# Kernel optimization log

Hardware: AMD Instinct MI355X
Metric: run time of the kernel (lower is better)

Reference implementation:

```python
import jax, jax.numpy as jnp
import numpy as np

H = 128   # d_model / features
N = 32    # kept complex modes (d_state=64 -> 32 conjugate pairs)
B = 8
L = 8192


def setup_inputs() -> dict:
    key = jax.random.key(0)
    ks = jax.random.split(key, 8)
    x = jax.random.normal(ks[0], (B, H, L), jnp.float32)
    # S4D (diagonal SSM) kernel parameters; channels=2 for bidirectional
    C_re = (jax.random.normal(ks[1], (2, H, N), jnp.float32) * (0.5 ** 0.5))
    C_im = (jax.random.normal(ks[2], (2, H, N), jnp.float32) * (0.5 ** 0.5))
    log_A_real = jnp.log(0.5 * jnp.ones((H, N), jnp.float32))          # S4D-Lin init
    A_imag = jnp.tile(np.pi * jnp.arange(N, dtype=jnp.float32), (H, 1))
    # log_dt uniform in [log(1e-3), log(1e-1)]
    u = jax.random.uniform(ks[3], (H,), jnp.float32)
    log_dt = u * (np.log(0.1) - np.log(0.001)) + np.log(0.001)
    D = jax.random.normal(ks[4], (H,), jnp.float32)                    # skip term
    W_pw = jax.random.normal(ks[5], (H, H), jnp.float32) / np.sqrt(H)  # 1x1 conv weight (out, in)
    gamma = jnp.ones((H,), jnp.float32)
    beta = jnp.zeros((H,), jnp.float32)
    return {"x": x, "C_re": C_re, "C_im": C_im, "log_A_real": log_A_real,
            "A_imag": A_imag, "log_dt": log_dt, "D": D, "W_pw": W_pw,
            "gamma": gamma, "beta": beta}


def reference(x, C_re, C_im, log_A_real, A_imag, log_dt, D, W_pw, gamma, beta):
    Lx = x.shape[-1]
    # ---- S4D SSM kernel via Vandermonde (ZOH discretization) ----
    A = -jnp.exp(log_A_real) + 1j * A_imag                 # (H, N) complex
    dt = jnp.exp(log_dt)[:, None]                          # (H, 1)
    dtA = A * dt                                           # (H, N)
    C = C_re + 1j * C_im                                   # (2, H, N)
    Kc = C * ((jnp.exp(dtA) - 1.0) / A)                    # (2, H, N)
    vand = jnp.exp(dtA[:, :, None] * jnp.arange(Lx))       # (H, N, L)
    k = 2.0 * jnp.einsum('chn,hnl->chl', Kc, vand).real    # (2, H, L)
    # ---- bidirectional: causal half + anticausal (flipped) half ----
    k_full = (jnp.pad(k[0], ((0, 0), (0, Lx)))
              + jnp.pad(k[1][:, ::-1], ((0, 0), (Lx, 0))))  # (H, 2L)
    # ---- FFT convolution ----
    n = 2 * Lx
    y = jnp.fft.irfft(jnp.fft.rfft(x, n=n) * jnp.fft.rfft(k_full, n=n), n=n)[..., :Lx]
    y = y + x * D[:, None]                                 # skip connection
    y = jax.nn.gelu(y, approximate=False)                  # FFTConv default activation
    # ---- pointwise 1x1 conv (no bias) ----
    y = jnp.einsum('bhl,oh->bol', y, W_pw)
    # ---- BatchNorm1d (training-mode batch statistics) ----
    mean = jnp.mean(y, axis=(0, 2), keepdims=True)
    var = jnp.var(y, axis=(0, 2), keepdims=True)
    y = (y - mean) * jax.lax.rsqrt(var + 1e-5) * gamma[:, None] + beta[:, None]
    # ---- ELU + residual (dropout p=0) ----
    return jax.nn.elu(y) + x
```

## Files before the change

### kernel.cpp

```cpp
#include <hip/hip_runtime.h>
#include <math.h>

#define HCH   128
#define NMODE 32
#define BB    8
#define LLEN  8192
#define LC    256
#define CCH   (LLEN / LC)
#define ROWS  (BB * HCH)

typedef unsigned int uint;
typedef _Float16 f16x8 __attribute__((ext_vector_type(8)));
typedef float    f32x4 __attribute__((ext_vector_type(4)));

static __device__ __forceinline__ uint pk2(float a, float b) {
    union { _Float16 h[2]; uint u; } v;
    v.h[0] = (_Float16)a; v.h[1] = (_Float16)b;
    return v.u;
}

static __device__ __forceinline__ void cpow8(float wr, float wi, int e, float& pr, float& pi) {
    pr = 1.f; pi = 0.f;
    float br = wr, bi = wi;
    #pragma unroll
    for (int k = 0; k < 8; k++) {
        if (e & (1 << k)) { float t = pr * br - pi * bi; pi = pr * bi + pi * br; pr = t; }
        float t2 = br * br - bi * bi; bi = 2.f * br * bi; br = t2;
    }
}

__device__ __forceinline__ float gelu_f(float y) {
    float z = fabsf(y) * 0.7071067811865476f;
    float p = fmaf(z, 0.078108f, 0.000972f);
    p = fmaf(z, p, 0.230389f);
    p = fmaf(z, p, 0.278393f);
    p = fmaf(z, p, 1.0f);
    float p2 = p * p;
    float p4 = p2 * p2;
    float er = 1.f - __builtin_amdgcn_rcpf(p4);
    float s  = copysignf(er, y);
    return 0.5f * y * (1.f + s);
}

#define DPP_ADD(v, ctrl) { int _t = __builtin_amdgcn_update_dpp(0, __float_as_int(v), \
                             (ctrl), 0xF, 0xF, true); (v) += __int_as_float(_t); }

__global__ __launch_bounds__(256) void k_prep(const float* __restrict__ C_re,
                                              const float* __restrict__ C_im,
                                              const float* __restrict__ logA,
                                              const float* __restrict__ Aim,
                                              const float* __restrict__ logdt,
                                              _Float16* __restrict__ aT,
                                              _Float16* __restrict__ eT,
                                              float* __restrict__ Pw,
                                              float* __restrict__ stats) {
    __shared__ float wrL[32], wiL[32];
    __shared__ float G0r[32], G0i[32], G1r[32], G1i[32], H0r[32], H0i[32];
    __shared__ float k0L[256], k1L[256];
    int tid = threadIdx.x;
    int h = blockIdx.x;
    if (blockIdx.x == 0) stats[tid] = 0.f;
    if (tid < 32) {
        int n = tid, idx = h * 32 + n;
        float ar = expf(logA[idx]);
        float ai = Aim[idx];
        float dt = expf(logdt[h]);
        float dre = -ar * dt, dim = ai * dt;
        float er = expf(dre);
        float wr = er * cosf(dim), wi = er * sinf(dim);
        wrL[n] = wr; wiL[n] = wi;
        float eL = expf(dre * 256.f);
        Pw[idx]        = eL * cosf(dim * 256.f);
        Pw[4096 + idx] = eL * sinf(dim * 256.f);
        float den  = ar * ar + ai * ai;
        float numr = -(wr - 1.f) * ar + wi * ai;
        float numi = -wi * ar - (wr - 1.f) * ai;
        float Kr = numr / den, Ki = numi / den;
        float c0r = C_re[idx],        c0i = C_im[idx];
        float c1r = C_re[4096 + idx], c1i = C_im[4096 + idx];
        float g0r = 2.f * (c0r * Kr - c0i * Ki), g0i = 2.f * (c0r * Ki + c0i * Kr);
        G0r[n] = g0r; G0i[n] = g0i;
        G1r[n] = 2.f * (c1r * Kr - c1i * Ki);
        G1i[n] = 2.f * (c1r * Ki + c1i * Kr);
        H0r[n] = g0r * wr - g0i * wi;
        H0i[n] = g0r * wi + g0i * wr;
    }
    __syncthreads();
    {
        int tau = tid;
        float s0 = 0.f, s1 = 0.f;
        for (int n = 0; n < 32; n++) {
            float pr, pi2; cpow8(wrL[n], wiL[n], tau, pr, pi2);
            s0 += G0r[n] * pr - G0i[n] * pi2;
            s1 += G1r[n] * pr - G1i[n] * pi2;
        }
        k0L[tau] = s0; k1L[tau] = s1;
    }
    __syncthreads();
    for (int idx = tid; idx < 256 * 128; idx += 256) {
        int t  = idx >> 7;
        int sp = (idx & 127) << 1;
        float v0 = (sp     <= t) ? k0L[t - sp]     : k1L[sp - t - 1];
        float v1 = (sp + 1 <= t) ? k0L[t - sp - 1] : k1L[sp - t];
        *(uint*)&aT[((size_t)(h * 256 + t)) * 384 + sp] = pk2(v0, v1);
    }
    {
        int t = tid;
        size_t rb = ((size_t)(h * 256 + t)) * 384;
        for (int n = 0; n < 32; n++) {
            float wtr, wti, wur, wui;
            cpow8(wrL[n], wiL[n], t, wtr, wti);
            cpow8(wrL[n], wiL[n], 255 - t, wur, wui);
            float v0r = H0r[n] * wtr - H0i[n] * wti;
            float v0i = -(H0r[n] * wti + H0i[n] * wtr);
            float v1r = G1r[n] * wur - G1i[n] * wui;
            float v1i = -(G1r[n] * wui + G1i[n] * wur);
            *(uint*)&aT[rb + 256 + 2 * n] = pk2(v0r, v0i);
            *(uint*)&aT[rb + 320 + 2 * n] = pk2(v1r, v1i);
        }
    }
    for (int idx = tid; idx < 32 * 256; idx += 256) {
        int n = idx >> 8, s = idx & 255;
        float ar, ai2, br, bi2;
        cpow8(wrL[n], wiL[n], 255 - s, ar, ai2);
        cpow8(wrL[n], wiL[n], s, br, bi2);
        size_t base = (size_t)h * 128 * 256;
        eT[base + (size_t)(2 * n) * 256 + s]      = (_Float16)ar;
        eT[base + (size_t)(2 * n + 1) * 256 + s]  = (_Float16)ai2;
        eT[base + (size_t)(64 + 2 * n) * 256 + s] = (_Float16)br;
        eT[base + (size_t)(65 + 2 * n) * 256 + s] = (_Float16)bi2;
    }
}

__global__ __launch_bounds__(256, 2) void k_states_g(const float* __restrict__ x,
                                                     const _Float16* __restrict__ eT,
                                                     float* __restrict__ S_end) {
    __shared__ _Float16 At[128 * 40];
    __shared__ _Float16 Bt[128 * 40];
    int tid = threadIdx.x;
    int bid = blockIdx.x;
    int h = bid >> 1, mt = bid & 1;
    int wave = tid >> 6, lane = tid & 63;
    int wm = wave >> 1, wn = wave & 1;
    int lrow = lane & 15, quad = lane >> 4;
    int koff = quad * 8;
    f32x4 acc[4][4];
    #pragma unroll
    for (int a = 0; a < 4; a++)
        #pragma unroll
        for (int b = 0; b < 4; b++) acc[a][b] = (f32x4){0.f, 0.f, 0.f, 0.f};

    for (int kk = 0; kk < 256; kk += 32) {
        __syncthreads();
        #pragma unroll
        for (int i = 0; i < 4; i++) {
            int idx = tid + i * 256;
            int r = idx >> 3, seg = idx & 7;
            int bc = mt * 128 + r;
            const float* xp = x + (((size_t)((bc >> 5) * HCH + h)) << 13) + ((bc & 31) << 8) + kk + seg * 4;
            float4 v = *(const float4*)xp;
            uint2 o; o.x = pk2(v.x, v.y); o.y = pk2(v.z, v.w);
            *(uint2*)&At[r * 40 + seg * 4] = o;
        }
        #pragma unroll
        for (int i = 0; i < 2; i++) {
            int idx = tid + i * 256;
            int r = idx >> 2, sg = idx & 3;
            uint4 v = *(const uint4*)(eT + ((size_t)(h * 128 + r)) * 256 + kk + sg * 8);
            *(uint4*)&Bt[r * 40 + sg * 8] = v;
        }
        __syncthreads();
        f16x8 a[4], b[4];
        #pragma unroll
        for (int f = 0; f < 4; f++) {
            a[f] = *(const f16x8*)&At[(wm * 64 + f * 16 + lrow) * 40 + koff];
            b[f] = *(const f16x8*)&Bt[(wn * 64 + f * 16 + lrow) * 40 + koff];
        }
        #pragma unroll
        for (int fi = 0; fi < 4; fi++)
            #pragma unroll
            for (int fj = 0; fj < 4; fj++)
                acc[fi][fj] = __builtin_amdgcn_mfma_f32_16x16x32_f16(a[fi], b[fj], acc[fi][fj], 0, 0, 0);
    }
    #pragma unroll
    for (int fi = 0; fi < 4; fi++) {
        #pragma unroll
        for (int fj = 0; fj < 4; fj++) {
            int srow = wn * 64 + fj * 16 + lrow;
            #pragma unroll
            for (int rg = 0; rg < 4; rg++) {
                int bc = mt * 128 + wm * 64 + fi * 16 + quad * 4 + rg;
                S_end[((size_t)(h * 256 + bc)) * 128 + srow] = acc[fi][fj][rg];
            }
        }
    }
}

__global__ void k_carries(const float* __restrict__ S_end, const float* __restrict__ Pw,
                          _Float16* __restrict__ carr) {
    int i = blockIdx.x * 256 + threadIdx.x;
    int n = i & 31; int d = (i >> 5) & 1; int row = i >> 6;
    int h = row & (HCH - 1), b = row >> 7;
    int pi = h * NMODE + n;
    float wLr = Pw[pi], wLi = Pw[4096 + pi];
    int srow = d * 64 + 2 * n;
    float cr = 0.f, ci = 0.f;
    if (d == 0) {
        for (int c = 0; c < CCH; c++) {
            size_t base = ((size_t)(h * 256 + b * 32 + c)) * 128 + srow;
            carr[base] = (_Float16)cr; carr[base + 1] = (_Float16)ci;
            float sr = S_end[base], si = S_end[base + 1];
            float nr = fmaf(wLr, cr, -wLi * ci) + sr;
            float ni = fmaf(wLi, cr,  wLr * ci) + si;
            cr = nr; ci = ni;
        }
    } else {
        for (int c = CCH - 1; c >= 0; c--) {
            size_t base = ((size_t)(h * 256 + b * 32 + c)) * 128 + srow;
            carr[base] = (_Float16)cr; carr[base + 1] = (_Float16)ci;
            float sr = S_end[base], si = S_end[base + 1];
            float nr = fmaf(wLr, cr, -wLi * ci) + sr;
            float ni = fmaf(wLi, cr,  wLr * ci) + si;
            cr = nr; ci = ni;
        }
    }
}

__global__ __launch_bounds__(256, 2) void k_conv_g(const float* __restrict__ x,
                                                   const _Float16* __restrict__ aT,
                                                   const _Float16* __restrict__ carr,
                                                   const float* __restrict__ D,
                                                   _Float16* __restrict__ Yg) {
    __shared__ _Float16 At[128 * 40];
    __shared__ _Float16 Bt[128 * 40];
    int tid = threadIdx.x;
    int bid = blockIdx.x;
    int h = bid >> 2, mt = (bid >> 1) & 1, nt = bid & 1;
    int wave = tid >> 6, lane = tid & 63;
    int wm = wave >> 1, wn = wave & 1;
    int lrow = lane & 15, quad = lane >> 4;
    int koff = quad * 8;
    f32x4 acc[4][4];
    #pragma unroll
    for (int a = 0; a < 4; a++)
        #pragma unroll
        for (int b = 0; b < 4; b++) acc[a][b] = (f32x4){0.f, 0.f, 0.f, 0.f};

    for (int kk = 0; kk < 384; kk += 32) {
        __syncthreads();
        if (kk < 256) {
            #pragma unroll
            for (int i = 0; i < 4; i++) {
                int idx = tid + i * 256;
                int r = idx >> 3, seg = idx & 7;
                int bc = mt * 128 + r;
                const float* xp = x + (((size_t)((bc >> 5) * HCH + h)) << 13) + ((bc & 31) << 8) + kk + seg * 4;
                float4 v = *(const float4*)xp;
                uint2 o; o.x = pk2(v.x, v.y); o.y = pk2(v.z, v.w);
                *(uint2*)&At[r * 40 + seg * 4] = o;
            }
        } else {
            #pragma unroll
            for (int i = 0; i < 2; i++) {
                int idx = tid + i * 256;
                int r = idx >> 2, sg = idx & 3;
                int bc = mt * 128 + r;
                uint4 v = *(const uint4*)(carr + ((size_t)(h * 256 + bc)) * 128 + (kk - 256) + sg * 8);
                *(uint4*)&At[r * 40 + sg * 8] = v;
            }
        }
        #pragma unroll
        for (int i = 0; i < 2; i++) {
            int idx = tid + i * 256;
            int r = idx >> 2, sg = idx & 3;
            int t = nt * 128 + r;
            uint4 v = *(const uint4*)(aT + ((size_t)(h * 256 + t)) * 384 + kk + sg * 8);
            *(uint4*)&Bt[r * 40 + sg * 8] = v;
        }
        __syncthreads();
        f16x8 a[4], b[4];
        #pragma unroll
        for (int f = 0; f < 4; f++) {
            a[f] = *(const f16x8*)&At[(wm * 64 + f * 16 + lrow) * 40 + koff];
            b[f] = *(const f16x8*)&Bt[(wn * 64 + f * 16 + lrow) * 40 + koff];
        }
        #pragma unroll
        for (int fi = 0; fi < 4; fi++)
            #pragma unroll
            for (int fj = 0; fj < 4; fj++)
                acc[fi][fj] = __builtin_amdgcn_mfma_f32_16x16x32_f16(a[fi], b[fj], acc[fi][fj], 0, 0, 0);
    }
    float Dh = D[h];
    #pragma unroll
    for (int fi = 0; fi < 4; fi++) {
        #pragma unroll
        for (int fj = 0; fj < 4; fj++) {
            int t = nt * 128 + wn * 64 + fj * 16 + lrow;
            #pragma unroll
            for (int rg = 0; rg < 4; rg++) {
                int bc = mt * 128 + wm * 64 + fi * 16 + quad * 4 + rg;
                size_t base = (((size_t)((bc >> 5) * HCH + h)) << 13) + ((bc & 31) << 8) + t;
                float xv = x[base];
                float yv = acc[fi][fj][rg] + Dh * xv;
                Yg[base] = (_Float16)gelu_f(yv);
            }
        }
    }
}

__global__ __launch_bounds__(256, 2) void k_pointwise(const _Float16* __restrict__ Yg,
                                                      const float* __restrict__ W,
                                                      float* __restrict__ z,
                                                      float* __restrict__ stats) {
    __shared__ _Float16 Wt[128 * 40];
    __shared__ _Float16 Yt[128 * 40];
    int tid = threadIdx.x;
    int b  = blockIdx.x >> 6;
    int l0 = (blockIdx.x & 63) << 7;
    int wave = tid >> 6, lane = tid & 63;
    int wm = wave >> 1, wn = wave & 1;
    int lrow = lane & 15, quad = lane >> 4;
    int koff = quad * 8;
    f32x4 acc[4][4];
    #pragma unroll
    for (int a = 0; a < 4; a++)
        #pragma unroll
        for (int c = 0; c < 4; c++) acc[a][c] = (f32x4){0.f, 0.f, 0.f, 0.f};

    for (int kk = 0; kk < 128; kk += 32) {
        __syncthreads();
        #pragma unroll
        for (int i = 0; i < 4; i++) {
            int idx = tid + i * 256;
            int r = idx >> 3, seg = idx & 7;
            float4 v = *(const float4*)(W + r * HCH + kk + seg * 4);
            uint2 o2; o2.x = pk2(v.x, v.y); o2.y = pk2(v.z, v.w);
            *(uint2*)&Wt[r * 40 + seg * 4] = o2;
        }
        #pragma unroll
        for (int i = 0; i < 2; i++) {
            int idx = tid + i * 256;
            int hh = idx & 31, lg = idx >> 5;
            uint4 v = *(const uint4*)(Yg + (((size_t)(b * HCH + kk + hh)) << 13) + l0 + lg * 8);
            const _Float16* hv = (const _Float16*)&v;
            #pragma unroll
            for (int j = 0; j < 8; j++)
                Yt[(lg * 8 + j) * 40 + hh] = hv[j];
        }
        __syncthreads();
        f16x8 a[4], bf[4];
        #pragma unroll
        for (int f = 0; f < 4; f++) {
            a[f]  = *(const f16x8*)&Wt[(wm * 64 + f * 16 + lrow) * 40 + koff];
            bf[f] = *(const f16x8*)&Yt[(wn * 64 + f * 16 + lrow) * 40 + koff];
        }
        #pragma unroll
        for (int fi = 0; fi < 4; fi++)
            #pragma unroll
            for (int fj = 0; fj < 4; fj++)
                acc[fi][fj] = __builtin_amdgcn_mfma_f32_16x16x32_f16(a[fi], bf[fj], acc[fi][fj], 0, 0, 0);
    }
    #pragma unroll
    for (int fi = 0; fi < 4; fi++) {
        #pragma unroll
        for (int fj = 0; fj < 4; fj++) {
            int l = l0 + wn * 64 + fj * 16 + lrow;
            #pragma unroll
            for (int rg = 0; rg < 4; rg++) {
                int o = wm * 64 + fi * 16 + quad * 4 + rg;
                z[(((size_t)(b * HCH + o)) << 13) + l] = acc[fi][fj][rg];
            }
        }
    }
    __syncthreads();
    float* Ls = (float*)Wt;
    #pragma unroll
    for (int fi = 0; fi < 4; fi++) {
        #pragma unroll
        for (int rg = 0; rg < 4; rg++) {
            float s = 0.f, q = 0.f;
            #pragma unroll
            for (int fj = 0; fj < 4; fj++) {
                float v = acc[fi][fj][rg];
                s += v; q = fmaf(v, v, q);
            }
            DPP_ADD(s, 0xB1); DPP_ADD(s, 0x4E); DPP_ADD(s, 0x141); DPP_ADD(s, 0x140);
            DPP_ADD(q, 0xB1); DPP_ADD(q, 0x4E); DPP_ADD(q, 0x141); DPP_ADD(q, 0x140);
            if (lrow == 0) {
                int olo = fi * 16 + quad * 4 + rg;
                Ls[wave * 64 + olo]       = s;
                Ls[256 + wave * 64 + olo] = q;
            }
        }
    }
    __syncthreads();
    if (tid < HCH) {
        int wmn = tid >> 6;
        int olo = tid & 63;
        float s = Ls[(wmn * 2) * 64 + olo] + Ls[(wmn * 2 + 1) * 64 + olo];
        float q = Ls[256 + (wmn * 2) * 64 + olo] + Ls[256 + (wmn * 2 + 1) * 64 + olo];
        atomicAdd(&stats[tid], s);
        atomicAdd(&stats[HCH + tid], q);
    }
}

__global__ __launch_bounds__(256) void k_final(const float* __restrict__ z,
                                               const float* __restrict__ x,
                                               const float* __restrict__ stats,
                                               const float* __restrict__ gamma,
                                               const float* __restrict__ beta,
                                               float* __restrict__ out) {
    size_t i4 = (size_t)blockIdx.x * 256 + threadIdx.x;
    if (i4 >= (size_t)BB * HCH * LLEN / 4) return;
    size_t flat = i4 * 4;
    int o = (int)((flat / LLEN) & (HCH - 1));
    const float inv_cnt = 1.f / (float)(BB * LLEN);
    float m   = stats[o] * inv_cnt;
    float var = stats[HCH + o] * inv_cnt - m * m;
    float rs  = rsqrtf(var + 1e-5f);
    float ga  = gamma[o] * rs;
    float bt  = beta[o] - m * ga;
    float4 zv = ((const float4*)z)[i4];
    float4 xv = ((const float4*)x)[i4];
    float4 r;
    { float t = fmaf(zv.x, ga, bt); float e = t > 0.f ? t : (__expf(t) - 1.f); r.x = e + xv.x; }
    { float t = fmaf(zv.y, ga, bt); float e = t > 0.f ? t : (__expf(t) - 1.f); r.y = e + xv.y; }
    { float t = fmaf(zv.z, ga, bt); float e = t > 0.f ? t : (__expf(t) - 1.f); r.z = e + xv.z; }
    { float t = fmaf(zv.w, ga, bt); float e = t > 0.f ? t : (__expf(t) - 1.f); r.w = e + xv.w; }
    ((float4*)out)[i4] = r;
}

extern "C" void kernel_launch(void* const* d_in, const int* in_sizes, int n_in,
                              void* d_out, int out_size, void* d_ws, size_t ws_size,
                              hipStream_t stream) {
    const float* x     = (const float*)d_in[0];
    const float* C_re  = (const float*)d_in[1];
    const float* C_im  = (const float*)d_in[2];
    const float* logA  = (const float*)d_in[3];
    const float* Aim   = (const float*)d_in[4];
    const float* logdt = (const float*)d_in[5];
    const float* D     = (const float*)d_in[6];
    const float* W     = (const float*)d_in[7];
    const float* gamma = (const float*)d_in[8];
    const float* beta  = (const float*)d_in[9];

    float* ws = (float*)d_ws;
    _Float16* eT    = (_Float16*)ws;
    float*    S_end = ws + 2097152;
    _Float16* Yg    = (_Float16*)ws;
    float*    zbuf  = ws + 8388608;
    _Float16* aT    = (_Float16*)zbuf;
    _Float16* carr  = (_Float16*)(ws + 16777216);
    float*    Pw    = ws + 16777216 + 2097152;
    float*    stats = Pw + 8192;
    float*    out   = (float*)d_out;

    k_prep     <<<128,  256, 0, stream>>>(C_re, C_im, logA, Aim, logdt, aT, eT, Pw, stats);
    k_states_g <<<256,  256, 0, stream>>>(x, eT, S_end);
    k_carries  <<<256,  256, 0, stream>>>(S_end, Pw, carr);
    k_conv_g   <<<512,  256, 0, stream>>>(x, aT, carr, D, Yg);
    k_pointwise<<<512,  256, 0, stream>>>(Yg, W, zbuf, stats);
    k_final    <<<8192, 256, 0, stream>>>(zbuf, x, stats, gamma, beta, out);
}
```

Measured before the change: 209.7 us.

## Precompute complex power table in shared memory and split prep kernel per channel

The prep kernel no longer computes each w^t with a per-element binary exponentiation. It builds a 32x256 table of powers in LDS once, using strided recurrences, and the kernel-tap, aT and eT construction loops read from that table. The grid is doubled so each channel is split across two blocks, each writing half of the time rows, which gives more parallelism. Each block recomputes the table redundantly, and the recurrence-based powers may accumulate slightly more rounding error than direct exponentiation.

```diff
diff --git a/kernel.cpp b/kernel.cpp
--- a/kernel.cpp
+++ b/kernel.cpp
@@ -17,16 +17,6 @@
     union { _Float16 h[2]; uint u; } v;
     v.h[0] = (_Float16)a; v.h[1] = (_Float16)b;
     return v.u;
-}
-
-static __device__ __forceinline__ void cpow8(float wr, float wi, int e, float& pr, float& pi) {
-    pr = 1.f; pi = 0.f;
-    float br = wr, bi = wi;
-    #pragma unroll
-    for (int k = 0; k < 8; k++) {
-        if (e & (1 << k)) { float t = pr * br - pi * bi; pi = pr * bi + pi * br; pr = t; }
-        float t2 = br * br - bi * bi; bi = 2.f * br * bi; br = t2;
-    }
 }
 
 __device__ __forceinline__ float gelu_f(float y) {
@@ -54,11 +44,14 @@
                                               _Float16* __restrict__ eT,
                                               float* __restrict__ Pw,
                                               float* __restrict__ stats) {
-    __shared__ float wrL[32], wiL[32];
-    __shared__ float G0r[32], G0i[32], G1r[32], G1i[32], H0r[32], H0i[32];
+    __shared__ float2 PL[32 * 257];
+    __shared__ float4 G01[32];
+    __shared__ float4 HG[32];
+    __shared__ float2 WL[32];
     __shared__ float k0L[256], k1L[256];
-    int tid = threadIdx.x;
-    int h = blockIdx.x;
+    int tid  = threadIdx.x;
+    int h    = blockIdx.x >> 1;
+    int half = blockIdx.x & 1;
     if (blockIdx.x == 0) stats[tid] = 0.f;
     if (tid < 32) {
         int n = tid, idx = h * 32 + n;
@@ -68,10 +61,12 @@
         float dre = -ar * dt, dim = ai * dt;
         float er = expf(dre);
         float wr = er * cosf(dim), wi = er * sinf(dim);
-        wrL[n] = wr; wiL[n] = wi;
-        float eL = expf(dre * 256.f);
-        Pw[idx]        = eL * cosf(dim * 256.f);
-        Pw[4096 + idx] = eL * sinf(dim * 256.f);
+        WL[n] = (float2){wr, wi};
+        if (half == 0) {
+            float eL = expf(dre * 256.f);
+            Pw[idx]        = eL * cosf(dim * 256.f);
+            Pw[4096 + idx] = eL * sinf(dim * 256.f);
+        }
         float den  = ar * ar + ai * ai;
         float numr = -(wr - 1.f) * ar + wi * ai;
         float numi = -wi * ar - (wr - 1.f) * ai;
@@ -79,56 +74,78 @@
         float c0r = C_re[idx],        c0i = C_im[idx];
         float c1r = C_re[4096 + idx], c1i = C_im[4096 + idx];
         float g0r = 2.f * (c0r * Kr - c0i * Ki), g0i = 2.f * (c0r * Ki + c0i * Kr);
-        G0r[n] = g0r; G0i[n] = g0i;
-        G1r[n] = 2.f * (c1r * Kr - c1i * Ki);
-        G1i[n] = 2.f * (c1r * Ki + c1i * Kr);
-        H0r[n] = g0r * wr - g0i * wi;
-        H0i[n] = g0r * wi + g0i * wr;
+        float g1r = 2.f * (c1r * Kr - c1i * Ki);
+        float g1i = 2.f * (c1r * Ki + c1i * Kr);
+        G01[n] = (float4){g0r, g0i, g1r, g1i};
+        HG[n]  = (float4){g0r * wr - g0i * wi, g0r * wi + g0i * wr, g1r, g1i};
+    }
+    __syncthreads();
+    {
+        int n = tid & 31, tg = tid >> 5;
+        float2 w = WL[n];
+        float w2r = w.x * w.x - w.y * w.y,   w2i = 2.f * w.x * w.y;
+        float w4r = w2r * w2r - w2i * w2i,   w4i = 2.f * w2r * w2i;
+        float w8r = w4r * w4r - w4i * w4i,   w8i = 2.f * w4r * w4i;
+        float pr = (tg & 1) ? w.x : 1.f;
+        float pi = (tg & 1) ? w.y : 0.f;
+        if (tg & 2) { float t2 = pr * w2r - pi * w2i; pi = pr * w2i + pi * w2r; pr = t2; }
+        if (tg & 4) { float t4 = pr * w4r - pi * w4i; pi = pr * w4i + pi * w4r; pr = t4; }
+        float2* row = &PL[n * 257];
+        #pragma unroll
+        for (int j = 0; j < 32; j++) {
+            row[tg + 8 * j] = (float2){pr, pi};
+            float tr = pr * w8r - pi * w8i; pi = pr * w8i + pi * w8r; pr = tr;
+        }
     }
     __syncthreads();
     {
         int tau = tid;
         float s0 = 0.f, s1 = 0.f;
+        #pragma unroll
         for (int n = 0; n < 32; n++) {
-            float pr, pi2; cpow8(wrL[n], wiL[n], tau, pr, pi2);
-            s0 += G0r[n] * pr - G0i[n] * pi2;
-            s1 += G1r[n] * pr - G1i[n] * pi2;
+            float2 p = PL[n * 257 + tau];
+            float4 g = G01[n];
+            s0 += g.x * p.x - g.y * p.y;
+            s1 += g.z * p.x - g.w * p.y;
         }
         k0L[tau] = s0; k1L[tau] = s1;
     }
     __syncthreads();
-    for (int idx = tid; idx < 256 * 128; idx += 256) {
-        int t  = idx >> 7;
+    #pragma unroll 4
+    for (int i = 0; i < 64; i++) {
+        int idx = i * 256 + tid;
+        int t  = half * 128 + (idx >> 7);
         int sp = (idx & 127) << 1;
         float v0 = (sp     <= t) ? k0L[t - sp]     : k1L[sp - t - 1];
         float v1 = (sp + 1 <= t) ? k0L[t - sp - 1] : k1L[sp - t];
         *(uint*)&aT[((size_t)(h * 256 + t)) * 384 + sp] = pk2(v0, v1);
     }
-    {
-        int t = tid;
+    #pragma unroll 4
+    for (int i = 0; i < 16; i++) {
+        int idx = i * 256 + tid;
+        int n = idx & 31;
+        int t = half * 128 + (idx >> 5);
+        float2 pt = PL[n * 257 + t];
+        float2 pu = PL[n * 257 + 255 - t];
+        float4 hg = HG[n];
         size_t rb = ((size_t)(h * 256 + t)) * 384;
-        for (int n = 0; n < 32; n++) {
-            float wtr, wti, wur, wui;
-            cpow8(wrL[n], wiL[n], t, wtr, wti);
-            cpow8(wrL[n], wiL[n], 255 - t, wur, wui);
-            float v0r = H0r[n] * wtr - H0i[n] * wti;
-            float v0i = -(H0r[n] * wti + H0i[n] * wtr);
-            float v1r = G1r[n] * wur - G1i[n] * wui;
-            float v1i = -(G1r[n] * wui + G1i[n] * wur);
-            *(uint*)&aT[rb + 256 + 2 * n] = pk2(v0r, v0i);
-            *(uint*)&aT[rb + 320 + 2 * n] = pk2(v1r, v1i);
-        }
-    }
-    for (int idx = tid; idx < 32 * 256; idx += 256) {
-        int n = idx >> 8, s = idx & 255;
-        float ar, ai2, br, bi2;
-        cpow8(wrL[n], wiL[n], 255 - s, ar, ai2);
-        cpow8(wrL[n], wiL[n], s, br, bi2);
+        *(uint*)&aT[rb + 256 + 2 * n] = pk2(hg.x * pt.x - hg.y * pt.y,
+                                            -(hg.x * pt.y + hg.y * pt.x));
+        *(uint*)&aT[rb + 320 + 2 * n] = pk2(hg.z * pu.x - hg.w * pu.y,
+                                            -(hg.z * pu.y + hg.w * pu.x));
+    }
+    #pragma unroll 4
+    for (int i = 0; i < 16; i++) {
+        int idx = i * 256 + tid;
+        int n = idx >> 7;
+        int s = half * 128 + (idx & 127);
+        float2 ps = PL[n * 257 + s];
+        float2 pu = PL[n * 257 + 255 - s];
         size_t base = (size_t)h * 128 * 256;
-        eT[base + (size_t)(2 * n) * 256 + s]      = (_Float16)ar;
-        eT[base + (size_t)(2 * n + 1) * 256 + s]  = (_Float16)ai2;
-        eT[base + (size_t)(64 + 2 * n) * 256 + s] = (_Float16)br;
-        eT[base + (size_t)(65 + 2 * n) * 256 + s] = (_Float16)bi2;
+        eT[base + (size_t)(2 * n) * 256 + s]      = (_Float16)pu.x;
+        eT[base + (size_t)(2 * n + 1) * 256 + s]  = (_Float16)pu.y;
+        eT[base + (size_t)(64 + 2 * n) * 256 + s] = (_Float16)ps.x;
+        eT[base + (size_t)(65 + 2 * n) * 256 + s] = (_Float16)ps.y;
     }
 }
 
@@ -455,7 +472,7 @@
     float*    stats = Pw + 8192;
     float*    out   = (float*)d_out;
 
-    k_prep     <<<128,  256, 0, stream>>>(C_re, C_im, logA, Aim, logdt, aT, eT, Pw, stats);
+    k_prep     <<<256,  256, 0, stream>>>(C_re, C_im, logA, Aim, logdt, aT, eT, Pw, stats);
     k_states_g <<<256,  256, 0, stream>>>(x, eT, S_end);
     k_carries  <<<256,  256, 0, stream>>>(S_end, Pw, carr);
     k_conv_g   <<<512,  256, 0, stream>>>(x, aT, carr, D, Yg);
```

Measured after the change: 187.9 us. 10.4% less time.
